# Optimization experiments

Measured on AMD Instinct MI355X. Metric: run time of the kernel, lower is better.

The kernel has to match this reference:

```python
import jax, jax.numpy as jnp
import numpy as np

N_NODES = 100000
N_EDGES = 1600000
IN_F = 128
OUT_F = 32


def setup_inputs() -> dict:
    key = jax.random.key(0)
    k1, k2, k3, k4, k5 = jax.random.split(key, 5)
    x = jax.random.normal(k1, (N_NODES, IN_F), dtype=jnp.float32)
    edge_row = jax.random.randint(k2, (N_EDGES,), 0, N_NODES, dtype=jnp.int64 if jax.config.jax_enable_x64 else jnp.int32)
    edge_col = jax.random.randint(k3, (N_EDGES,), 0, N_NODES, dtype=jnp.int64 if jax.config.jax_enable_x64 else jnp.int32)
    edge_val = jax.random.uniform(k4, (N_EDGES,), dtype=jnp.float32)
    # Xavier-normal init like nn.init.xavier_normal_
    std = float(np.sqrt(2.0 / (IN_F + OUT_F)))
    weight = jax.random.normal(k5, (IN_F, OUT_F), dtype=jnp.float32) * std
    bias = jnp.zeros((OUT_F,), dtype=jnp.float32)
    return {"x": x, "edge_row": edge_row, "edge_col": edge_col,
            "edge_val": edge_val, "weight": weight, "bias": bias}


def reference(x, edge_row, edge_col, edge_val, weight, bias):
    # support = x @ W  (dense GEMM)
    support = x @ weight  # [N, out]
    # output = adj @ support, adj in COO form: out[row] += val * support[col]
    gathered = support[edge_col] * edge_val[:, None]  # [E, out]
    output = jax.ops.segment_sum(gathered, edge_row, num_segments=N_NODES)
    return output + bias
```

## Files before the change

kernel.cpp:

```cpp
#include <hip/hip_runtime.h>
#include <hip/hip_bf16.h>

#define N_NODES 100000
#define N_EDGES 1600000
#define IN_F 128
#define OUT_F 32

#define NBK 782
#define CAP 3392
#define TILE_A 3125
#define NWG_A 512
#define NWG_G 98
#define OVCAP 4096

typedef float v4f __attribute__((ext_vector_type(4)));
typedef short bf16x8 __attribute__((ext_vector_type(8)));
typedef float f32x4 __attribute__((ext_vector_type(4)));

__device__ inline unsigned short f2bf(float f) {
  unsigned u = __float_as_uint(f);
  return (unsigned short)((u + 0x7FFFu + ((u >> 16) & 1u)) >> 16);
}
__device__ inline float bf2f(unsigned short h) {
  return __uint_as_float(((unsigned)h) << 16);
}
__device__ inline unsigned pk2(float lo, float hi) {
  return (unsigned)f2bf(lo) | ((unsigned)f2bf(hi) << 16);
}

__global__ __launch_bounds__(1024) void gcn_fused_kernel(
    const float* __restrict__ x, const float* __restrict__ w,
    unsigned short* __restrict__ sup, const int* __restrict__ erow,
    const int* __restrict__ ecol, const float* __restrict__ eval,
    int* __restrict__ cursor, int* __restrict__ ovcnt, int4* __restrict__ ov,
    int2* __restrict__ bedges) {
  __shared__ int h[NBK];
  __shared__ int gbase[NBK];
  __shared__ int lcur[NBK];
  const int t = threadIdx.x;

  if (blockIdx.x < NWG_G) {
    const int wid = t >> 6;
    const int lane = t & 63;
    const int lr = lane & 15;
    const int lg = lane >> 4;
    const int wrow0 = blockIdx.x * 1024 + wid * 64;

    bf16x8 bfrag[2][4];
    #pragma unroll
    for (int nt = 0; nt < 2; ++nt) {
      #pragma unroll
      for (int kk = 0; kk < 4; ++kk) {
        const int c = nt * 16 + lr;
        const int k0 = kk * 32 + lg * 8;
        union { unsigned u[4]; bf16x8 v; } bf;
        #pragma unroll
        for (int d = 0; d < 4; ++d)
          bf.u[d] = pk2(w[(k0 + 2 * d) * OUT_F + c],
                        w[(k0 + 2 * d + 1) * OUT_F + c]);
        bfrag[nt][kk] = bf.v;
      }
    }

    f32x4 acc[4][2];
    #pragma unroll
    for (int m = 0; m < 4; ++m) { acc[m][0] = 0.f; acc[m][1] = 0.f; }

    #pragma unroll
    for (int m = 0; m < 4; ++m) {
      const int row = wrow0 + m * 16 + lr;
      const int rl = (row < N_NODES) ? row : (N_NODES - 1);
      const float* xr = x + (size_t)rl * IN_F;
      #pragma unroll
      for (int kk = 0; kk < 4; ++kk) {
        const v4f p0 = *(const v4f*)(xr + kk * 32 + lg * 8);
        const v4f p1 = *(const v4f*)(xr + kk * 32 + lg * 8 + 4);
        union { unsigned u[4]; bf16x8 v; } af;
        af.u[0] = pk2(p0.x, p0.y);
        af.u[1] = pk2(p0.z, p0.w);
        af.u[2] = pk2(p1.x, p1.y);
        af.u[3] = pk2(p1.z, p1.w);
        acc[m][0] = __builtin_amdgcn_mfma_f32_16x16x32_bf16(af.v, bfrag[0][kk], acc[m][0], 0, 0, 0);
        acc[m][1] = __builtin_amdgcn_mfma_f32_16x16x32_bf16(af.v, bfrag[1][kk], acc[m][1], 0, 0, 0);
      }
    }
    #pragma unroll
    for (int m = 0; m < 4; ++m) {
      #pragma unroll
      for (int i = 0; i < 4; ++i) {
        const int r = wrow0 + m * 16 + lg * 4 + i;
        if (r < N_NODES) {
          sup[((size_t)r << 5) + lr] = f2bf(acc[m][0][i]);
          sup[((size_t)r << 5) + 16 + lr] = f2bf(acc[m][1][i]);
        }
      }
    }
  } else {
    const int base = (blockIdx.x - NWG_G) * TILE_A;
    const int lim = base + TILE_A;
    for (int i = t; i < NBK; i += 1024) { h[i] = 0; lcur[i] = 0; }
    __syncthreads();
    int rowv[4];
    #pragma unroll
    for (int i = 0; i < 4; ++i) {
      const int e = base + i * 1024 + t;
      rowv[i] = (e < lim) ? erow[e] : -1;
      if (rowv[i] >= 0) atomicAdd(&h[rowv[i] >> 7], 1);
    }
    __syncthreads();
    if (t < NBK) {
      const int c = h[t];
      gbase[t] = c ? atomicAdd(&cursor[t], (c + 3) & ~3) : 0;
    }
    __syncthreads();
    #pragma unroll
    for (int i = 0; i < 4; ++i) {
      if (rowv[i] >= 0) {
        const int e = base + i * 1024 + t;
        const int r = rowv[i];
        const int b = r >> 7;
        const int k = atomicAdd(&lcur[b], 1);
        const int pos = gbase[b] + k;
        const int2 pk = make_int2(ecol[e] | ((r & 127) << 17),
                                  __float_as_int(eval[e]));
        if (pos < CAP) {
          bedges[(size_t)b * CAP + pos] = pk;
        } else {
          const int o = atomicAdd(ovcnt, 1);
          if (o < OVCAP) ov[o] = make_int4(b, pk.x, pk.y, 0);
        }
      }
    }
    __syncthreads();
    if (t < NBK) {
      const int c = h[t];
      const int resv = (c + 3) & ~3;
      for (int j = c; j < resv; ++j) {
        const int pos = gbase[t] + j;
        if (pos < CAP) bedges[(size_t)t * CAP + pos] = make_int2(0, 0);
      }
    }
  }
}

__global__ __launch_bounds__(1024) void gcn_gather_kernel(
    const unsigned short* __restrict__ sup, const int* __restrict__ cursor,
    const int2* __restrict__ bedges, const int* __restrict__ ovcnt,
    const int4* __restrict__ ov, const float* __restrict__ bias,
    float* __restrict__ out) {
  __shared__ int2 stage[CAP];
  __shared__ int2 sorted[CAP];
  __shared__ int hist[128];
  __shared__ int csr[129];
  __shared__ int cur[128];
  const int t = threadIdx.x;
  const int b = blockIdx.x;
  const int f = t & 31;
  const int g = t >> 5;
  const int ext = min(cursor[b], CAP);
  const size_t bb = (size_t)b * CAP;
  float acc[4] = {0.f, 0.f, 0.f, 0.f};

  if (t < 128) hist[t] = 0;
  __syncthreads();
  for (int j = t; j < ext; j += 1024) {
    const int2 ed = bedges[bb + j];
    stage[j] = ed;
    if (ed.y != 0) atomicAdd(&hist[(ed.x >> 17) & 127], 1);
  }
  __syncthreads();
  if (t < 64) {
    const int v0 = hist[2 * t];
    const int v1 = hist[2 * t + 1];
    int s = v0 + v1;
    #pragma unroll
    for (int off = 1; off < 64; off <<= 1) {
      const int up = __shfl_up(s, off, 64);
      if (t >= off) s += up;
    }
    const int excl = s - (v0 + v1);
    csr[2 * t] = excl;
    csr[2 * t + 1] = excl + v0;
    cur[2 * t] = excl;
    cur[2 * t + 1] = excl + v0;
    if (t == 63) csr[128] = s;
  }
  __syncthreads();
  for (int j = t; j < ext; j += 1024) {
    const int2 ed = stage[j];
    if (ed.y != 0) {
      const int k = atomicAdd(&cur[(ed.x >> 17) & 127], 1);
      sorted[k] = ed;
    }
  }
  __syncthreads();

  #pragma unroll
  for (int rr = 0; rr < 4; ++rr) {
    const int lr = g * 4 + rr;
    const int e1 = csr[lr + 1];
    int e = csr[lr];
    for (; e + 8 <= e1; e += 8) {
      const int2 q0 = sorted[e],     q1 = sorted[e + 1];
      const int2 q2 = sorted[e + 2], q3 = sorted[e + 3];
      const int2 q4 = sorted[e + 4], q5 = sorted[e + 5];
      const int2 q6 = sorted[e + 6], q7 = sorted[e + 7];
      const float v0 = bf2f(sup[((size_t)(q0.x & 0x1FFFF) << 5) + f]);
      const float v1 = bf2f(sup[((size_t)(q1.x & 0x1FFFF) << 5) + f]);
      const float v2 = bf2f(sup[((size_t)(q2.x & 0x1FFFF) << 5) + f]);
      const float v3 = bf2f(sup[((size_t)(q3.x & 0x1FFFF) << 5) + f]);
      const float v4 = bf2f(sup[((size_t)(q4.x & 0x1FFFF) << 5) + f]);
      const float v5 = bf2f(sup[((size_t)(q5.x & 0x1FFFF) << 5) + f]);
      const float v6 = bf2f(sup[((size_t)(q6.x & 0x1FFFF) << 5) + f]);
      const float v7 = bf2f(sup[((size_t)(q7.x & 0x1FFFF) << 5) + f]);
      acc[rr] += __int_as_float(q0.y) * v0 + __int_as_float(q1.y) * v1 +
                 __int_as_float(q2.y) * v2 + __int_as_float(q3.y) * v3 +
                 __int_as_float(q4.y) * v4 + __int_as_float(q5.y) * v5 +
                 __int_as_float(q6.y) * v6 + __int_as_float(q7.y) * v7;
    }
    for (; e + 4 <= e1; e += 4) {
      const int2 q0 = sorted[e],     q1 = sorted[e + 1];
      const int2 q2 = sorted[e + 2], q3 = sorted[e + 3];
      const float v0 = bf2f(sup[((size_t)(q0.x & 0x1FFFF) << 5) + f]);
      const float v1 = bf2f(sup[((size_t)(q1.x & 0x1FFFF) << 5) + f]);
      const float v2 = bf2f(sup[((size_t)(q2.x & 0x1FFFF) << 5) + f]);
      const float v3 = bf2f(sup[((size_t)(q3.x & 0x1FFFF) << 5) + f]);
      acc[rr] += __int_as_float(q0.y) * v0 + __int_as_float(q1.y) * v1 +
                 __int_as_float(q2.y) * v2 + __int_as_float(q3.y) * v3;
    }
    for (; e < e1; ++e) {
      const int2 q = sorted[e];
      acc[rr] += __int_as_float(q.y) *
                 bf2f(sup[((size_t)(q.x & 0x1FFFF) << 5) + f]);
    }
  }

  const int on = min(*ovcnt, OVCAP);
  for (int i = 0; i < on; ++i) {
    const int4 q = ov[i];
    if (q.x == b) {
      const int lr = (q.y >> 17) & 127;
      if ((lr >> 2) == g)
        acc[lr & 3] += __int_as_float(q.z) *
                       bf2f(sup[((size_t)(q.y & 0x1FFFF) << 5) + f]);
    }
  }

  const int row0 = b << 7;
  const float bv = bias[f];
  #pragma unroll
  for (int rr = 0; rr < 4; ++rr) {
    const int row = row0 + g * 4 + rr;
    if (row < N_NODES) out[((size_t)row << 5) + f] = acc[rr] + bv;
  }
}

__global__ __launch_bounds__(256) void gcn_gemm_fb_kernel(
    const float* __restrict__ x, const float* __restrict__ w,
    unsigned short* __restrict__ sup) {
  __shared__ float wlds[IN_F][OUT_F];
  const int t = threadIdx.x;
  for (int i = t; i < 1024; i += 256)
    ((float4*)wlds)[i] = ((const float4*)w)[i];
  __syncthreads();
  const int tr = t >> 3;
  const int c0 = (t & 7) * 4;
  const int row = blockIdx.x * 32 + tr;
  if (row >= N_NODES) return;
  const float* xr = x + (size_t)row * IN_F;
  v4f acc = 0.f;
  #pragma unroll 4
  for (int kb = 0; kb < IN_F; kb += 4) {
    const v4f xv = *(const v4f*)(xr + kb);
    acc += xv.x * *(const v4f*)&wlds[kb + 0][c0];
    acc += xv.y * *(const v4f*)&wlds[kb + 1][c0];
    acc += xv.z * *(const v4f*)&wlds[kb + 2][c0];
    acc += xv.w * *(const v4f*)&wlds[kb + 3][c0];
  }
  ushort4 o;
  o.x = f2bf(acc.x); o.y = f2bf(acc.y); o.z = f2bf(acc.z); o.w = f2bf(acc.w);
  *(ushort4*)(sup + ((size_t)row << 5) + c0) = o;
}

__global__ __launch_bounds__(256) void gcn_init_out_kernel(
    float* __restrict__ out, const float* __restrict__ bias) {
  const int i = blockIdx.x * 256 + threadIdx.x;
  if (i < N_NODES * OUT_F / 4)
    ((float4*)out)[i] = ((const float4*)bias)[i & 7];
}

__global__ __launch_bounds__(256) void gcn_scatter_kernel(
    const unsigned short* __restrict__ sup, const int* __restrict__ erow,
    const int* __restrict__ ecol, const float* __restrict__ eval,
    float* __restrict__ out) {
  const long long idx = (long long)blockIdx.x * 256 + threadIdx.x;
  if (idx >= (long long)N_EDGES * OUT_F) return;
  const int e = (int)(idx >> 5);
  const int ff = (int)(idx & 31);
  atomicAdd(&out[((size_t)erow[e] << 5) + ff],
            eval[e] * bf2f(sup[((size_t)ecol[e] << 5) + ff]));
}

extern "C" void kernel_launch(void* const* d_in, const int* in_sizes, int n_in,
                              void* d_out, int out_size, void* d_ws, size_t ws_size,
                              hipStream_t stream) {
  const float* x = (const float*)d_in[0];
  const int* erow = (const int*)d_in[1];
  const int* ecol = (const int*)d_in[2];
  const float* eval = (const float*)d_in[3];
  const float* w = (const float*)d_in[4];
  const float* bias = (const float*)d_in[5];
  float* out = (float*)d_out;
  char* ws = (char*)d_ws;

  const size_t SUP_OFF = 0;
  const size_t CUR_OFF = SUP_OFF + 6400000;
  const size_t OVC_OFF = CUR_OFF + 3128;
  const size_t OV_OFF  = CUR_OFF + 3200;
  const size_t BED_OFF = OV_OFF + 65536;
  const size_t NEEDED  = BED_OFF + (size_t)NBK * CAP * 8;

  unsigned short* sup = (unsigned short*)(ws + SUP_OFF);

  if (ws_size >= NEEDED) {
    int* cursor = (int*)(ws + CUR_OFF);
    int* ovcnt  = (int*)(ws + OVC_OFF);
    int4* ov    = (int4*)(ws + OV_OFF);
    int2* bedges = (int2*)(ws + BED_OFF);

    hipMemsetAsync(cursor, 0, 3132, stream);
    gcn_fused_kernel<<<NWG_G + NWG_A, 1024, 0, stream>>>(
        x, w, sup, erow, ecol, eval, cursor, ovcnt, ov, bedges);
    gcn_gather_kernel<<<NBK, 1024, 0, stream>>>(
        sup, cursor, bedges, ovcnt, ov, bias, out);
  } else if (ws_size >= 6400000) {
    gcn_gemm_fb_kernel<<<(N_NODES + 31) / 32, 256, 0, stream>>>(x, w, sup);
    gcn_init_out_kernel<<<(N_NODES * OUT_F / 4 + 255) / 256, 256, 0, stream>>>(out, bias);
    const long long total = (long long)N_EDGES * OUT_F;
    gcn_scatter_kernel<<<(int)((total + 255) / 256), 256, 0, stream>>>(
        sup, erow, ecol, eval, out);
  }
}
```

Baseline: 72.01 us.

## Stage bucketed edges in LDS and write them out contiguously per bucket

The bucketing phase now prefix-sums per-bucket counts inside the workgroup, stages packed edges in shared memory grouped by bucket, then writes them to global memory in bucket order, so the stores land in contiguous runs instead of being scattered. The padding of each reservation to a multiple of four is dropped, along with its zero-fill pass. Tile size grows to 4096 edges per workgroup, which means fewer workgroups, and CAP shrinks. The gather kernel, which is not shown, may still assume reservations padded to four entries, so correctness depends on that code, and the smaller CAP raises the chance of overflow.

```diff
diff --git a/kernel.cpp b/kernel.cpp
--- a/kernel.cpp
+++ b/kernel.cpp
@@ -7,9 +7,9 @@
 #define OUT_F 32
 
 #define NBK 782
-#define CAP 3392
-#define TILE_A 3125
-#define NWG_A 512
+#define CAP 2816
+#define TILE_A 4096
+#define NWG_A 391
 #define NWG_G 98
 #define OVCAP 4096
 
@@ -34,7 +34,10 @@
     const int* __restrict__ ecol, const float* __restrict__ eval,
     int* __restrict__ cursor, int* __restrict__ ovcnt, int4* __restrict__ ov,
     int2* __restrict__ bedges) {
+  __shared__ int2 stage[TILE_A];
+  __shared__ int dstg[TILE_A];
   __shared__ int h[NBK];
+  __shared__ int lstart[NBK];
   __shared__ int gbase[NBK];
   __shared__ int lcur[NBK];
   const int t = threadIdx.x;
@@ -97,48 +100,76 @@
     }
   } else {
     const int base = (blockIdx.x - NWG_G) * TILE_A;
-    const int lim = base + TILE_A;
+    const int tot = min(TILE_A, N_EDGES - base);
     for (int i = t; i < NBK; i += 1024) { h[i] = 0; lcur[i] = 0; }
     __syncthreads();
-    int rowv[4];
+
+    int rowv[4], colv[4];
+    float valv[4];
     #pragma unroll
     for (int i = 0; i < 4; ++i) {
       const int e = base + i * 1024 + t;
-      rowv[i] = (e < lim) ? erow[e] : -1;
-      if (rowv[i] >= 0) atomicAdd(&h[rowv[i] >> 7], 1);
+      if (e < N_EDGES) {
+        rowv[i] = erow[e]; colv[i] = ecol[e]; valv[i] = eval[e];
+        atomicAdd(&h[rowv[i] >> 7], 1);
+      } else rowv[i] = -1;
     }
     __syncthreads();
+
+    if (t < 64) {
+      const int b0 = t * 13;
+      int vals[13];
+      int s = 0;
+      #pragma unroll
+      for (int i = 0; i < 13; ++i) {
+        const int b = b0 + i;
+        vals[i] = (b < NBK) ? h[b] : 0;
+        s += vals[i];
+      }
+      int ssum = s;
+      #pragma unroll
+      for (int off = 1; off < 64; off <<= 1) {
+        const int up = __shfl_up(ssum, off, 64);
+        if (t >= off) ssum += up;
+      }
+      int excl = ssum - s;
+      #pragma unroll
+      for (int i = 0; i < 13; ++i) {
+        const int b = b0 + i;
+        if (b < NBK) { lstart[b] = excl; excl += vals[i]; }
+      }
+    }
     if (t < NBK) {
       const int c = h[t];
-      gbase[t] = c ? atomicAdd(&cursor[t], (c + 3) & ~3) : 0;
+      gbase[t] = c ? atomicAdd(&cursor[t], c) : 0;
     }
     __syncthreads();
+
     #pragma unroll
     for (int i = 0; i < 4; ++i) {
       if (rowv[i] >= 0) {
-        const int e = base + i * 1024 + t;
         const int r = rowv[i];
         const int b = r >> 7;
         const int k = atomicAdd(&lcur[b], 1);
-        const int pos = gbase[b] + k;
-        const int2 pk = make_int2(ecol[e] | ((r & 127) << 17),
-                                  __float_as_int(eval[e]));
-        if (pos < CAP) {
-          bedges[(size_t)b * CAP + pos] = pk;
+        const int idx = lstart[b] + k;
+        const int lo = colv[i] | ((r & 127) << 17);
+        const int hi = __float_as_int(valv[i]);
+        stage[idx] = make_int2(lo, hi);
+        const int dst = gbase[b] + k;
+        if (dst < CAP) {
+          dstg[idx] = b * CAP + dst;
         } else {
+          dstg[idx] = -1;
           const int o = atomicAdd(ovcnt, 1);
-          if (o < OVCAP) ov[o] = make_int4(b, pk.x, pk.y, 0);
+          if (o < OVCAP) ov[o] = make_int4(b, lo, hi, 0);
         }
       }
     }
     __syncthreads();
-    if (t < NBK) {
-      const int c = h[t];
-      const int resv = (c + 3) & ~3;
-      for (int j = c; j < resv; ++j) {
-        const int pos = gbase[t] + j;
-        if (pos < CAP) bedges[(size_t)t * CAP + pos] = make_int2(0, 0);
-      }
+
+    for (int j = t; j < tot; j += 1024) {
+      const int d = dstg[j];
+      if (d >= 0) bedges[d] = stage[j];
     }
   }
 }
```

New measurement: 66.63 us. -7.5%, faster.
